# Optimization experiments

Measured on AMD Instinct MI355X. Metric: run time of the kernel, lower is better.

The kernel has to match this reference:

```python
import jax, jax.numpy as jnp
import numpy as np

NX = 65536   # spatial cells
T = 32       # time points
H = 128      # MLP hidden width
DX = 1.0     # spatial resolution (init kwarg dx)
S0, S1 = -1.0, 1.0  # fixed stencil (learn_stencil=False)


def setup_inputs() -> dict:
    key = jax.random.key(0)
    k1, k2, k3, k4 = jax.random.split(key, 4)
    t = jnp.arange(T, dtype=jnp.float32) * 0.01          # time grid, dt=0.01
    u0 = jax.random.uniform(k1, (NX,), jnp.float32)      # initial state
    inv_sqrt_h = jnp.float32(1.0 / np.sqrt(H))
    W1 = jax.random.normal(k2, (1, H), jnp.float32)
    W2 = jax.random.normal(k3, (H, H), jnp.float32) * inv_sqrt_h
    W3 = jax.random.normal(k4, (H, 1), jnp.float32) * inv_sqrt_h
    D = jnp.full((1,), 0.01, jnp.float32)                # diffusion coefficient
    BC = jnp.zeros((2, 1), jnp.float32)                  # Dirichlet BC values
    return {"t": t, "u0": u0, "W1": W1, "W2": W2, "W3": W3, "D": D, "BC": BC}


def _flux(u, W1, W2, W3, D, BC):
    # per-cell MLP (func_nn): Linear->Tanh->Linear->Tanh->Linear, no bias, no sigmoid
    h = jnp.tanh(u[:, None] @ W1)        # [Nx, H]
    h = jnp.tanh(h @ W2)                 # [Nx, H]
    a = (h @ W3)[:, 0]                   # [Nx]
    a_plus = jax.nn.relu(a)
    a_min = -jax.nn.relu(-a)
    d = D[0]
    # left fluxes
    lb = d * (S0 * u[0] + S1 * BC[0, 0]) - a_plus[0] / DX * (-S0 * u[0] - S1 * BC[0, 0])
    ln = d * (S0 * u[1:] + S1 * u[:-1]) - a_plus[1:] / DX * (-S0 * u[1:] - S1 * u[:-1])
    left = jnp.concatenate([lb[None], ln])
    # right fluxes
    rb = d * (S0 * u[-1] + S1 * BC[1, 0]) - a_min[-1] / DX * (S0 * u[-1] + S1 * BC[1, 0])
    rn = d * (S0 * u[:-1] + S1 * u[1:]) - a_min[:-1] / DX * (S0 * u[:-1] + S1 * u[1:])
    right = jnp.concatenate([rn, rb[None]])
    return left + right


def reference(t, u0, W1, W2, W3, D, BC):
    # Neural-ODE integration of du/dt = flux_kernel(u); fixed-step RK4 over grid t
    f = lambda u: _flux(u, W1, W2, W3, D, BC)

    def step(u, dt):
        k1 = f(u)
        k2 = f(u + 0.5 * dt * k1)
        k3 = f(u + 0.5 * dt * k2)
        k4 = f(u + dt * k3)
        un = u + (dt / 6.0) * (k1 + 2.0 * k2 + 2.0 * k3 + k4)
        return un, un

    _, us = jax.lax.scan(step, u0, jnp.diff(t))
    return jnp.concatenate([u0[None], us], axis=0)  # [T, Nx]
```

## Files before the change

### kernel.cpp

```cpp
#include <hip/hip_runtime.h>

#define NXC 65536
#define TT 32
#define HH 128
#define TABN 6145
#define TABNP 6146
#define TABLO (-1.0f)
#define TABINV 2048.0f
#define OUTW 32
#define VC 2
#define WINW 128
#define HALO 48

typedef __attribute__((ext_vector_type(8))) short bf16x8;
typedef __attribute__((ext_vector_type(4))) float f32x4;
typedef unsigned short u16;

__device__ __forceinline__ float bf2f(u16 b) {
    union { unsigned int u; float f; } v; v.u = ((unsigned int)b) << 16; return v.f;
}
__device__ __forceinline__ u16 f2bf(float f) {
    union { float f; unsigned int u; } v; v.f = f;
    return (u16)((v.u + 0x7fffu + ((v.u >> 16) & 1u)) >> 16);
}
__device__ __forceinline__ bool is_bf16_mode(const void* t) {
    return ((const u16*)t)[1] != 0;
}

#if __has_builtin(__builtin_amdgcn_exp2f)
#define EXP2F(x) __builtin_amdgcn_exp2f(x)
#else
#define EXP2F(x) exp2f(x)
#endif
#if __has_builtin(__builtin_amdgcn_rcpf)
#define RCPF(x) __builtin_amdgcn_rcpf(x)
#else
#define RCPF(x) (1.0f / (x))
#endif

__device__ __forceinline__ float fast_tanh(float x) {
    float e = EXP2F(x * 2.8853900817779268f);
    return 1.0f - 2.0f * RCPF(e + 1.0f);
}

__global__ void w2swz_kernel(const void* t, const void* W2,
                             u16* __restrict__ w2frag) {
    bool bf = is_bf16_mode(t);
    int i = blockIdx.x * 256 + threadIdx.x;
    int j = i & 7;
    int lane = (i >> 3) & 63;
    int ks = (i >> 9) & 3;
    int nt = i >> 11;
    int k = ks * 32 + (lane >> 4) * 8 + j;
    int n = nt * 16 + (lane & 15);
    w2frag[i] = bf ? ((const u16*)W2)[k * HH + n]
                   : f2bf(((const float*)W2)[k * HH + n]);
}

__global__ __launch_bounds__(256) void tabbuild_kernel(
    const void* traw, const void* W1, const void* W3,
    const u16* __restrict__ w2frag, float* __restrict__ atab) {
    __shared__ float w1s[HH];
    __shared__ float w3s[HH];
    bool bf = is_bf16_mode(traw);
    int tid = threadIdx.x;
    if (tid < HH)
        w1s[tid] = bf ? bf2f(((const u16*)W1)[tid]) : ((const float*)W1)[tid];
    else
        w3s[tid - HH] = bf ? bf2f(((const u16*)W3)[tid - HH])
                           : ((const float*)W3)[tid - HH];
    __syncthreads();

    int lane = tid & 63;
    int wave = tid >> 6;
    int q = lane >> 4;
    int m = lane & 15;
    int base = (blockIdx.x * 4 + wave) * 16;
    float uin = TABLO + (float)(base + m) * (1.0f / TABINV);

    bf16x8 afrag[4];
#pragma unroll
    for (int ks = 0; ks < 4; ++ks)
#pragma unroll
        for (int j = 0; j < 8; ++j) {
            float h = fast_tanh(uin * w1s[ks * 32 + q * 8 + j]);
            afrag[ks][j] = (short)f2bf(h);
        }

    const bf16x8* w2f = (const bf16x8*)w2frag;
    float p0 = 0.f, p1 = 0.f, p2 = 0.f, p3 = 0.f;
#pragma unroll
    for (int nt = 0; nt < 8; ++nt) {
        f32x4 acc = {0.f, 0.f, 0.f, 0.f};
#pragma unroll
        for (int ks = 0; ks < 4; ++ks) {
            bf16x8 b = w2f[(nt * 4 + ks) * 64 + lane];
            acc = __builtin_amdgcn_mfma_f32_16x16x32_bf16(afrag[ks], b, acc, 0, 0, 0);
        }
        float w3v = w3s[nt * 16 + m];
        p0 += fast_tanh(acc[0]) * w3v;
        p1 += fast_tanh(acc[1]) * w3v;
        p2 += fast_tanh(acc[2]) * w3v;
        p3 += fast_tanh(acc[3]) * w3v;
    }
#pragma unroll
    for (int sh = 1; sh < 16; sh <<= 1) {
        p0 += __shfl_xor(p0, sh, 64);
        p1 += __shfl_xor(p1, sh, 64);
        p2 += __shfl_xor(p2, sh, 64);
        p3 += __shfl_xor(p3, sh, 64);
    }
    int r = m & 3;
    float a = (r == 0) ? p0 : (r == 1) ? p1 : (r == 2) ? p2 : p3;
    if (m < 4) {
        int e = base + q * 4 + r;
        if (e < TABNP) atab[e] = a;
    }
}

__global__ void u0cvt_kernel(const void* t, const void* u0,
                             float* __restrict__ u, void* out) {
    bool bf = is_bf16_mode(t);
    int i = blockIdx.x * 256 + threadIdx.x;
    if (bf) {
        u16 v = ((const u16*)u0)[i];
        u[i] = bf2f(v);
        ((u16*)out)[i] = v;
    } else {
        float v = ((const float*)u0)[i];
        u[i] = v;
        ((float*)out)[i] = v;
    }
}

__global__ __launch_bounds__(256) void chunk_kernel(
    const void* traw, const float* __restrict__ uin, float* __restrict__ uout,
    const void* Draw, const void* BCraw, const float* __restrict__ atab,
    void* outbase, int s0, int nsteps) {
    __shared__ float2 tab[TABN];
    __shared__ float t32s[TT];

    int tid = threadIdx.x;
    bool bf = is_bf16_mode(traw);
    for (int i = tid; i < TABN; i += 256) {
        float v0 = atab[i];
        float v1 = atab[i + 1];
        tab[i] = make_float2(v0, v1 - v0);
    }
    if (tid < TT)
        t32s[tid] = bf ? bf2f(((const u16*)traw)[tid]) : ((const float*)traw)[tid];

    float d   = bf ? bf2f(((const u16*)Draw)[0])  : ((const float*)Draw)[0];
    float bc0 = bf ? bf2f(((const u16*)BCraw)[0]) : ((const float*)BCraw)[0];
    float bc1 = bf ? bf2f(((const u16*)BCraw)[1]) : ((const float*)BCraw)[1];

    int lane = tid & 63;
    int wid = blockIdx.x * 4 + (tid >> 6);
    int o0 = wid * OUTW;
    int wsg = o0 - HALO;
    int gb = wsg + lane * VC;
    int i0 = lane * VC;

    float v[VC], ub[VC], kacc[VC], kk[VC];
    bool gok[VC], isl[VC], isr[VC], own[VC];
#pragma unroll
    for (int j = 0; j < VC; ++j) {
        int g = gb + j;
        int i = i0 + j;
        gok[j] = (g >= 0) && (g < NXC);
        isl[j] = (g == 0);
        isr[j] = (g == NXC - 1);
        own[j] = (i >= HALO) && (i < HALO + OUTW);
        float x = gok[j] ? uin[g] : 0.f;
        v[j] = x;
        ub[j] = x;
    }
    __syncthreads();

    for (int st = 0; st < nsteps; ++st) {
        int step = s0 + st;
        float dt = t32s[step + 1] - t32s[step];
        float dt2 = 0.5f * dt, dt6 = dt * (1.0f / 6.0f);
#pragma unroll
        for (int j = 0; j < VC; ++j) kacc[j] = 0.f;
#pragma unroll
        for (int s = 0; s < 4; ++s) {
            int sigma = st * 4 + s;
            float cnext = (s < 2) ? dt2 : dt;
            float wgt = (s == 1 || s == 2) ? 2.f : 1.f;
            float vup = __shfl_up(v[VC - 1], 1, 64);
            float vdn = __shfl_down(v[0], 1, 64);
#pragma unroll
            for (int j = 0; j < VC; ++j) {
                float vc = v[j];
                float vl = (j == 0) ? vup : v[j - 1];
                float vr = (j == VC - 1) ? vdn : v[j + 1];
                vl = isl[j] ? bc0 : vl;
                vr = isr[j] ? bc1 : vr;
                float f = fmaf(vc, TABINV, (-TABLO) * TABINV);
                f = fminf(fmaxf(f, 0.0f), (float)(TABN - 1));
                int e0 = (int)f;
                float frac = f - (float)e0;
                float2 ts = tab[e0];
                float a = fmaf(frac, ts.y, ts.x);
                float ap = fmaxf(a, 0.f);
                float am = fminf(a, 0.f);
                float kv = (vl - vc) * (d + ap) + (vr - vc) * (d - am);
                int i = i0 + j;
                bool act = gok[j] && (i > sigma) && (i < WINW - 1 - sigma);
                kk[j] = act ? kv : 0.f;
            }
#pragma unroll
            for (int j = 0; j < VC; ++j) {
                int i = i0 + j;
                bool act = gok[j] && (i > sigma) && (i < WINW - 1 - sigma);
                kacc[j] += wgt * kk[j];
                if (act) {
                    if (s < 3) {
                        v[j] = fmaf(cnext, kk[j], ub[j]);
                    } else {
                        float vn = fmaf(dt6, kacc[j], ub[j]);
                        v[j] = vn;
                        ub[j] = vn;
                    }
                }
            }
        }
        size_t rb = (size_t)(step + 1) * NXC;
#pragma unroll
        for (int j = 0; j < VC; ++j) {
            if (own[j]) {
                if (bf) ((u16*)outbase)[rb + gb + j] = f2bf(ub[j]);
                else    ((float*)outbase)[rb + gb + j] = ub[j];
            }
        }
    }
#pragma unroll
    for (int j = 0; j < VC; ++j)
        if (own[j]) uout[gb + j] = ub[j];
}

extern "C" void kernel_launch(void* const* d_in, const int* in_sizes, int n_in,
                              void* d_out, int out_size, void* d_ws,
                              size_t ws_size, hipStream_t stream) {
    const void* t  = d_in[0];
    const void* u0 = d_in[1];
    const void* W1 = d_in[2];
    const void* W2 = d_in[3];
    const void* W3 = d_in[4];
    const void* Dp = d_in[5];
    const void* BC = d_in[6];

    float* atab = (float*)d_ws;
    u16* w2frag = (u16*)(atab + TABNP + 2);
    float* uA = (float*)(w2frag + 16384);
    float* uB = uA + NXC;

    w2swz_kernel<<<64, 256, 0, stream>>>(t, W2, w2frag);
    tabbuild_kernel<<<(TABNP + 63) / 64, 256, 0, stream>>>(t, W1, W3, w2frag, atab);
    u0cvt_kernel<<<NXC / 256, 256, 0, stream>>>(t, u0, uA, d_out);

    const int grid = NXC / (OUTW * 4);
    chunk_kernel<<<grid, 256, 0, stream>>>(t, uA, uB, Dp, BC, atab, d_out, 0, 12);
    chunk_kernel<<<grid, 256, 0, stream>>>(t, uB, uA, Dp, BC, atab, d_out, 12, 12);
    chunk_kernel<<<grid, 256, 0, stream>>>(t, uA, uB, Dp, BC, atab, d_out, 24, 7);
}
```

Baseline: 111.4 us.

## Fuse W2 swizzle and u0 conversion into other kernels, simplify stencil masking

Moves the W2 fragment swizzle into the table-build kernel through shared memory, and folds the u0 conversion and initial output row into the first chunk kernel. This removes two separate kernel launches. The inner RK4 loop drops per-stage halo activity masks: out-of-domain cells are seeded with the boundary values and simply not updated. Table staging and output stores are vectorised. The tabbuild kernel now reloads all of W2 in every block, and the correctness of the interior halo cells now depends on the halo width being large enough.

```diff
diff --git a/kernel.cpp b/kernel.cpp
--- a/kernel.cpp
+++ b/kernel.cpp
@@ -43,23 +43,10 @@
     return 1.0f - 2.0f * RCPF(e + 1.0f);
 }
 
-__global__ void w2swz_kernel(const void* t, const void* W2,
-                             u16* __restrict__ w2frag) {
-    bool bf = is_bf16_mode(t);
-    int i = blockIdx.x * 256 + threadIdx.x;
-    int j = i & 7;
-    int lane = (i >> 3) & 63;
-    int ks = (i >> 9) & 3;
-    int nt = i >> 11;
-    int k = ks * 32 + (lane >> 4) * 8 + j;
-    int n = nt * 16 + (lane & 15);
-    w2frag[i] = bf ? ((const u16*)W2)[k * HH + n]
-                   : f2bf(((const float*)W2)[k * HH + n]);
-}
-
 __global__ __launch_bounds__(256) void tabbuild_kernel(
-    const void* traw, const void* W1, const void* W3,
-    const u16* __restrict__ w2frag, float* __restrict__ atab) {
+    const void* traw, const void* W1, const void* W2, const void* W3,
+    float* __restrict__ atab) {
+    __shared__ __align__(16) u16 w2s[HH * HH];
     __shared__ float w1s[HH];
     __shared__ float w3s[HH];
     bool bf = is_bf16_mode(traw);
@@ -69,6 +56,14 @@
     else
         w3s[tid - HH] = bf ? bf2f(((const u16*)W3)[tid - HH])
                            : ((const float*)W3)[tid - HH];
+#pragma unroll 4
+    for (int it = 0; it < (HH * HH) / 256; ++it) {
+        int idx = it * 256 + tid;
+        u16 b = bf ? ((const u16*)W2)[idx] : f2bf(((const float*)W2)[idx]);
+        int k = idx >> 7, n = idx & 127;
+        int frag = ((n >> 4) * 4 + (k >> 5)) * 64 + ((k >> 3) & 3) * 16 + (n & 15);
+        w2s[(frag << 3) | (k & 7)] = b;
+    }
     __syncthreads();
 
     int lane = tid & 63;
@@ -87,7 +82,7 @@
             afrag[ks][j] = (short)f2bf(h);
         }
 
-    const bf16x8* w2f = (const bf16x8*)w2frag;
+    const bf16x8* w2f = (const bf16x8*)w2s;
     float p0 = 0.f, p1 = 0.f, p2 = 0.f, p3 = 0.f;
 #pragma unroll
     for (int nt = 0; nt < 8; ++nt) {
@@ -118,35 +113,26 @@
     }
 }
 
-__global__ void u0cvt_kernel(const void* t, const void* u0,
-                             float* __restrict__ u, void* out) {
-    bool bf = is_bf16_mode(t);
-    int i = blockIdx.x * 256 + threadIdx.x;
-    if (bf) {
-        u16 v = ((const u16*)u0)[i];
-        u[i] = bf2f(v);
-        ((u16*)out)[i] = v;
-    } else {
-        float v = ((const float*)u0)[i];
-        u[i] = v;
-        ((float*)out)[i] = v;
-    }
-}
-
 __global__ __launch_bounds__(256) void chunk_kernel(
-    const void* traw, const float* __restrict__ uin, float* __restrict__ uout,
+    const void* traw, const void* uin, float* __restrict__ uout,
     const void* Draw, const void* BCraw, const float* __restrict__ atab,
     void* outbase, int s0, int nsteps) {
-    __shared__ float2 tab[TABN];
+    __shared__ __align__(16) float2 tab[TABN];
     __shared__ float t32s[TT];
 
     int tid = threadIdx.x;
     bool bf = is_bf16_mode(traw);
-    for (int i = tid; i < TABN; i += 256) {
-        float v0 = atab[i];
-        float v1 = atab[i + 1];
-        tab[i] = make_float2(v0, v1 - v0);
-    }
+
+    for (int e = tid * 4; e < TABN - 1; e += 1024) {
+        float4 qv = *(const float4*)(atab + e);
+        float nx = atab[e + 4];
+        float4 lo = make_float4(qv.x, qv.y - qv.x, qv.y, qv.z - qv.y);
+        float4 hi = make_float4(qv.z, qv.w - qv.z, qv.w, nx - qv.w);
+        *(float4*)(&tab[e]) = lo;
+        *(float4*)(&tab[e + 2]) = hi;
+    }
+    if (tid == 0)
+        tab[TABN - 1] = make_float2(atab[TABN - 1], atab[TABN] - atab[TABN - 1]);
     if (tid < TT)
         t32s[tid] = bf ? bf2f(((const u16*)traw)[tid]) : ((const float*)traw)[tid];
 
@@ -156,22 +142,32 @@
 
     int lane = tid & 63;
     int wid = blockIdx.x * 4 + (tid >> 6);
-    int o0 = wid * OUTW;
-    int wsg = o0 - HALO;
-    int gb = wsg + lane * VC;
+    int gb = wid * OUTW - HALO + lane * VC;
     int i0 = lane * VC;
-
-    float v[VC], ub[VC], kacc[VC], kk[VC];
-    bool gok[VC], isl[VC], isr[VC], own[VC];
+    bool first = (s0 == 0);
+    bool ownw = (i0 >= HALO) && (i0 < HALO + OUTW);
+
+    float v[VC], ub[VC], kv[VC], kacc[VC];
+    bool gok[VC];
 #pragma unroll
     for (int j = 0; j < VC; ++j) {
         int g = gb + j;
-        int i = i0 + j;
         gok[j] = (g >= 0) && (g < NXC);
-        isl[j] = (g == 0);
-        isr[j] = (g == NXC - 1);
-        own[j] = (i >= HALO) && (i < HALO + OUTW);
-        float x = gok[j] ? uin[g] : 0.f;
+        float x;
+        if (first) {
+            if (bf) {
+                u16 raw = gok[j] ? ((const u16*)uin)[g] : (u16)0;
+                x = bf2f(raw);
+                if (ownw) ((u16*)outbase)[g] = raw;
+            } else {
+                float raw = gok[j] ? ((const float*)uin)[g] : 0.f;
+                x = raw;
+                if (ownw) ((float*)outbase)[g] = raw;
+            }
+        } else {
+            x = gok[j] ? ((const float*)uin)[g] : 0.f;
+        }
+        if (!gok[j]) x = (g < 0) ? bc0 : bc1;
         v[j] = x;
         ub[j] = x;
     }
@@ -185,7 +181,6 @@
         for (int j = 0; j < VC; ++j) kacc[j] = 0.f;
 #pragma unroll
         for (int s = 0; s < 4; ++s) {
-            int sigma = st * 4 + s;
             float cnext = (s < 2) ? dt2 : dt;
             float wgt = (s == 1 || s == 2) ? 2.f : 1.f;
             float vup = __shfl_up(v[VC - 1], 1, 64);
@@ -195,8 +190,6 @@
                 float vc = v[j];
                 float vl = (j == 0) ? vup : v[j - 1];
                 float vr = (j == VC - 1) ? vdn : v[j + 1];
-                vl = isl[j] ? bc0 : vl;
-                vr = isr[j] ? bc1 : vr;
                 float f = fmaf(vc, TABINV, (-TABLO) * TABINV);
                 f = fminf(fmaxf(f, 0.0f), (float)(TABN - 1));
                 int e0 = (int)f;
@@ -205,39 +198,32 @@
                 float a = fmaf(frac, ts.y, ts.x);
                 float ap = fmaxf(a, 0.f);
                 float am = fminf(a, 0.f);
-                float kv = (vl - vc) * (d + ap) + (vr - vc) * (d - am);
-                int i = i0 + j;
-                bool act = gok[j] && (i > sigma) && (i < WINW - 1 - sigma);
-                kk[j] = act ? kv : 0.f;
+                kv[j] = (vl - vc) * (d + ap) + (vr - vc) * (d - am);
             }
 #pragma unroll
             for (int j = 0; j < VC; ++j) {
-                int i = i0 + j;
-                bool act = gok[j] && (i > sigma) && (i < WINW - 1 - sigma);
-                kacc[j] += wgt * kk[j];
-                if (act) {
-                    if (s < 3) {
-                        v[j] = fmaf(cnext, kk[j], ub[j]);
-                    } else {
-                        float vn = fmaf(dt6, kacc[j], ub[j]);
-                        v[j] = vn;
-                        ub[j] = vn;
-                    }
+                kacc[j] += wgt * kv[j];
+                float nv = (s < 3) ? fmaf(cnext, kv[j], ub[j])
+                                   : fmaf(dt6, kacc[j], ub[j]);
+                if (gok[j]) {
+                    v[j] = nv;
+                    if (s == 3) ub[j] = nv;
                 }
             }
         }
-        size_t rb = (size_t)(step + 1) * NXC;
-#pragma unroll
-        for (int j = 0; j < VC; ++j) {
-            if (own[j]) {
-                if (bf) ((u16*)outbase)[rb + gb + j] = f2bf(ub[j]);
-                else    ((float*)outbase)[rb + gb + j] = ub[j];
-            }
-        }
-    }
-#pragma unroll
-    for (int j = 0; j < VC; ++j)
-        if (own[j]) uout[gb + j] = ub[j];
+        long long rb = (long long)(step + 1) * NXC + gb;
+        if (ownw) {
+            if (bf) {
+                unsigned int pk = (unsigned int)f2bf(ub[0])
+                                | ((unsigned int)f2bf(ub[1]) << 16);
+                *(unsigned int*)&((u16*)outbase)[rb] = pk;
+            } else {
+                *(float2*)&((float*)outbase)[rb] = make_float2(ub[0], ub[1]);
+            }
+        }
+    }
+    if (uout != nullptr && ownw)
+        *(float2*)&uout[gb] = make_float2(ub[0], ub[1]);
 }
 
 extern "C" void kernel_launch(void* const* d_in, const int* in_sizes, int n_in,
@@ -252,16 +238,13 @@
     const void* BC = d_in[6];
 
     float* atab = (float*)d_ws;
-    u16* w2frag = (u16*)(atab + TABNP + 2);
-    float* uA = (float*)(w2frag + 16384);
+    float* uA = atab + TABNP + 2;
     float* uB = uA + NXC;
 
-    w2swz_kernel<<<64, 256, 0, stream>>>(t, W2, w2frag);
-    tabbuild_kernel<<<(TABNP + 63) / 64, 256, 0, stream>>>(t, W1, W3, w2frag, atab);
-    u0cvt_kernel<<<NXC / 256, 256, 0, stream>>>(t, u0, uA, d_out);
+    tabbuild_kernel<<<(TABNP + 63) / 64, 256, 0, stream>>>(t, W1, W2, W3, atab);
 
     const int grid = NXC / (OUTW * 4);
-    chunk_kernel<<<grid, 256, 0, stream>>>(t, uA, uB, Dp, BC, atab, d_out, 0, 12);
+    chunk_kernel<<<grid, 256, 0, stream>>>(t, u0, uB, Dp, BC, atab, d_out, 0, 12);
     chunk_kernel<<<grid, 256, 0, stream>>>(t, uB, uA, Dp, BC, atab, d_out, 12, 12);
-    chunk_kernel<<<grid, 256, 0, stream>>>(t, uA, uB, Dp, BC, atab, d_out, 24, 7);
-}
+    chunk_kernel<<<grid, 256, 0, stream>>>(t, uA, nullptr, Dp, BC, atab, d_out, 24, 7);
+}
```

New measurement: 118.3 us. +6.3%, slower.
